# Kernel optimization log

Hardware: AMD Instinct MI355X
Metric: run time of the kernel (lower is better)

Reference implementation:

```python
import jax, jax.numpy as jnp
import numpy as np

IN_CH, OUT_CH, B, H, W = 32, 64, 8, 256, 256
EPS = 1e-5

SOBEL_X = [[1., 0., -1.], [2., 0., -2.], [1., 0., -1.]]
SOBEL_Y = [[1., 2., 1.], [0., 0., 0.], [-1., -2., -1.]]
LAP = [[0., 1., 0.], [1., -4., 1.], [0., 1., 0.]]

DN = ('NCHW', 'OIHW', 'NCHW')


def conv2d(x, w, b, pad, groups=1):
    y = jax.lax.conv_general_dilated(x, w, (1, 1), [(pad, pad), (pad, pad)],
                                     dimension_numbers=DN, feature_group_count=groups)
    return y + b[None, :, None, None]


def dw_conv(x, k2d):
    # fixed depthwise 3x3 conv, groups=C, padding=1, no bias
    c = x.shape[1]
    kern = jnp.tile(jnp.asarray(k2d, x.dtype)[None, None], (c, 1, 1, 1))  # (C,1,3,3)
    return jax.lax.conv_general_dilated(x, kern, (1, 1), [(1, 1), (1, 1)],
                                        dimension_numbers=DN, feature_group_count=c)


def bn4d(x, p):  # eval-mode BN; x (B,C,H,W), p (4,C) = gamma, beta, mean, var
    g, b, m, v = p
    s = g * jax.lax.rsqrt(v + EPS)
    return (x - m[None, :, None, None]) * s[None, :, None, None] + b[None, :, None, None]


def bn2d(h, p):  # h (B,C)
    g, b, m, v = p
    return (h - m) * (g * jax.lax.rsqrt(v + EPS)) + b


def _bn_params(key, c):
    k1, k2, k3, k4 = jax.random.split(key, 4)
    g = 1.0 + 0.1 * jax.random.normal(k1, (c,), jnp.float32)
    b = 0.1 * jax.random.normal(k2, (c,), jnp.float32)
    m = 0.1 * jax.random.normal(k3, (c,), jnp.float32)
    v = jax.random.uniform(k4, (c,), jnp.float32, 0.5, 1.5)
    return jnp.stack([g, b, m, v])


def setup_inputs() -> dict:
    key = jax.random.key(0)
    ks = jax.random.split(key, 24)
    s = 0.05
    return {
        'x': jax.random.normal(ks[0], (B, IN_CH, H, W), jnp.float32),
        'gate_w1': s * jax.random.normal(ks[1], (IN_CH, IN_CH), jnp.float32),
        'gate_b1': s * jax.random.normal(ks[2], (IN_CH,), jnp.float32),
        'gate_bn': _bn_params(ks[3], IN_CH),
        'gate_w2': s * jax.random.normal(ks[4], (3, IN_CH), jnp.float32),
        'gate_b2': s * jax.random.normal(ks[5], (3,), jnp.float32),
        'mw1': s * jax.random.normal(ks[6], (OUT_CH, IN_CH, 3, 3), jnp.float32),
        'mb1': s * jax.random.normal(ks[7], (OUT_CH,), jnp.float32),
        'mbn1': _bn_params(ks[8], OUT_CH),
        'mw2': s * jax.random.normal(ks[9], (OUT_CH, OUT_CH, 5, 5), jnp.float32),
        'mb2': s * jax.random.normal(ks[10], (OUT_CH,), jnp.float32),
        'mbn2': _bn_params(ks[11], OUT_CH),
        'sxw': s * jax.random.normal(ks[12], (OUT_CH, IN_CH, 5, 5), jnp.float32),
        'sxb': s * jax.random.normal(ks[13], (OUT_CH,), jnp.float32),
        'sxbn': _bn_params(ks[14], OUT_CH),
        'syw': s * jax.random.normal(ks[15], (OUT_CH, IN_CH, 5, 5), jnp.float32),
        'syb': s * jax.random.normal(ks[16], (OUT_CH,), jnp.float32),
        'sybn': _bn_params(ks[17], OUT_CH),
        'lw': s * jax.random.normal(ks[18], (OUT_CH, IN_CH, 5, 5), jnp.float32),
        'lb': s * jax.random.normal(ks[19], (OUT_CH,), jnp.float32),
        'lbn': _bn_params(ks[20], OUT_CH),
    }


def reference(x, gate_w1, gate_b1, gate_bn, gate_w2, gate_b2,
              mw1, mb1, mbn1, mw2, mb2, mbn2,
              sxw, sxb, sxbn, syw, syb, sybn, lw, lb, lbn):
    # gate: GAP -> 1x1 conv -> BN -> tanh -> 1x1 conv -> top-1 one-hot over 3 experts
    gap = x.mean((2, 3))                                   # (B, C_in)
    h = jnp.tanh(bn2d(gap @ gate_w1.T + gate_b1, gate_bn))
    k = h @ gate_w2.T + gate_b2                            # (B, 3)
    oh = jax.nn.one_hot(jnp.argmax(k, axis=1), 3, dtype=x.dtype)  # (B, 3)

    # expert 0: main branch (conv3x3+BN+ReLU -> conv5x5+BN+ReLU)
    main = jax.nn.relu(bn4d(conv2d(x, mw1, mb1, 1), mbn1))
    main = jax.nn.relu(bn4d(conv2d(main, mw2, mb2, 2), mbn2))

    # expert 1: mean of sobel-x and sobel-y branches
    sx = jax.nn.relu(bn4d(conv2d(dw_conv(x, SOBEL_X), sxw, sxb, 2), sxbn))
    sy = jax.nn.relu(bn4d(conv2d(dw_conv(x, SOBEL_Y), syw, syb, 2), sybn))
    sobel = (sx + sy) * 0.5

    # expert 2: laplacian branch
    lap = jax.nn.relu(bn4d(conv2d(dw_conv(x, LAP), lw, lb, 2), lbn))

    # one-hot gated combination (== stack + one_hot mask + sum in the original)
    w = oh[:, :, None, None, None]  # (B, 3, 1, 1, 1)
    return main * w[:, 0] + sobel * w[:, 1] + lap * w[:, 2]
```

## Files before the change

kernel.cpp:

```cpp
#include <hip/hip_runtime.h>

#define BB 8
#define IC 32
#define OC 64
#define HH 256
#define WW 256
#define EPS 1e-5f

typedef __attribute__((ext_vector_type(8))) short bf16x8;
typedef __attribute__((ext_vector_type(4))) float f32x4;

#define XSTR 40
#define YSTR 40

#define WS_GAP   0
#define WS_BIDX  256
#define WS_W1F   264
#define WS_B1F   (WS_W1F + 9216)
#define WS_W2F   (WS_B1F + 64)
#define WS_B2F   (WS_W2F + 51200)
#define WS_SXWT  (WS_B2F + 64)
#define WS_SXBF  (WS_SXWT + 51200)
#define WS_SYWT  (WS_SXBF + 64)
#define WS_SYBF  (WS_SYWT + 51200)
#define WS_LWT   (WS_SYBF + 64)
#define WS_LBF   (WS_LWT + 51200)

__device__ inline unsigned short bf16r(float f) {
    unsigned int u = __float_as_uint(f);
    unsigned int r = (u + 0x7fffu + ((u >> 16) & 1u)) >> 16;
    return (unsigned short)r;
}

__global__ void prep_kernel(const float* __restrict__ mw1, const float* __restrict__ mb1, const float* __restrict__ mbn1,
                            const float* __restrict__ mw2, const float* __restrict__ mb2, const float* __restrict__ mbn2,
                            const float* __restrict__ sxw, const float* __restrict__ sxb, const float* __restrict__ sxbn,
                            const float* __restrict__ syw, const float* __restrict__ syb, const float* __restrict__ sybn,
                            const float* __restrict__ lw,  const float* __restrict__ lb,  const float* __restrict__ lbn,
                            float* __restrict__ ws) {
    int idx = blockIdx.x * 256 + threadIdx.x;

    if (idx < 18432) {
        int j = idx & 7, lane = (idx >> 3) & 63, oct = (idx >> 9) & 1, ht = idx >> 10;
        int t = ht % 9, h = ht / 9;
        int oc = h * 32 + oct * 16 + (lane & 15);
        int ic = (lane >> 4) * 8 + j;
        float s = mbn1[oc] * rsqrtf(mbn1[192 + oc] + EPS);
        ((unsigned short*)(ws + WS_W1F))[idx] = bf16r(mw1[(oc * IC + ic) * 9 + t] * s);
    }
    if (idx < 102400) {
        int j = idx & 7, lane = (idx >> 3) & 63, oct = (idx >> 9) & 3, ht = idx >> 11;
        int t = ht % 25, h = ht / 25;
        int oc = oct * 16 + (lane & 15);
        int ic = h * 32 + (lane >> 4) * 8 + j;
        float s = mbn2[oc] * rsqrtf(mbn2[192 + oc] + EPS);
        ((unsigned short*)(ws + WS_W2F))[idx] = bf16r(mw2[(oc * OC + ic) * 25 + t] * s);
    }
    if (idx < 51200) {
        int oc = idx & 63, k = (idx >> 6) % 25, ic = idx / (25 * 64);
        float ssx = sxbn[oc] * rsqrtf(sxbn[192 + oc] + EPS);
        float ssy = sybn[oc] * rsqrtf(sybn[192 + oc] + EPS);
        float sl  = lbn[oc]  * rsqrtf(lbn[192 + oc]  + EPS);
        ws[WS_SXWT + idx] = sxw[(oc * IC + ic) * 25 + k] * ssx;
        ws[WS_SYWT + idx] = syw[(oc * IC + ic) * 25 + k] * ssy;
        ws[WS_LWT  + idx] = lw [(oc * IC + ic) * 25 + k] * sl;
    }
    if (idx < 64) {
        float s1 = mbn1[idx] * rsqrtf(mbn1[192 + idx] + EPS);
        ws[WS_B1F + idx] = (mb1[idx] - mbn1[128 + idx]) * s1 + mbn1[64 + idx];
        float s2 = mbn2[idx] * rsqrtf(mbn2[192 + idx] + EPS);
        ws[WS_B2F + idx] = (mb2[idx] - mbn2[128 + idx]) * s2 + mbn2[64 + idx];
        float sx = sxbn[idx] * rsqrtf(sxbn[192 + idx] + EPS);
        ws[WS_SXBF + idx] = (sxb[idx] - sxbn[128 + idx]) * sx + sxbn[64 + idx];
        float sy = sybn[idx] * rsqrtf(sybn[192 + idx] + EPS);
        ws[WS_SYBF + idx] = (syb[idx] - sybn[128 + idx]) * sy + sybn[64 + idx];
        float sl = lbn[idx] * rsqrtf(lbn[192 + idx] + EPS);
        ws[WS_LBF + idx] = (lb[idx] - lbn[128 + idx]) * sl + lbn[64 + idx];
    }
}

__global__ void gap_kernel(const float* __restrict__ x, float* __restrict__ ws) {
    int bc = blockIdx.x;
    const float4* p = (const float4*)(x + (size_t)bc * (HH * WW));
    float s = 0.f;
    for (int i = threadIdx.x; i < (HH * WW) / 4; i += 256) {
        float4 v = p[i];
        s += (v.x + v.y) + (v.z + v.w);
    }
    #pragma unroll
    for (int off = 32; off; off >>= 1) s += __shfl_down(s, off, 64);
    __shared__ float red[4];
    int lane = threadIdx.x & 63, w = threadIdx.x >> 6;
    if (lane == 0) red[w] = s;
    __syncthreads();
    if (threadIdx.x == 0)
        ws[WS_GAP + bc] = (red[0] + red[1] + red[2] + red[3]) * (1.f / (HH * WW));
}

__global__ void gate_kernel(const float* __restrict__ w1, const float* __restrict__ b1,
                            const float* __restrict__ gbn,
                            const float* __restrict__ w2, const float* __restrict__ b2,
                            float* __restrict__ ws) {
    __shared__ float hsh[8][32];
    int tid = threadIdx.x;
    int b = tid >> 5, j = tid & 31;
    float acc = b1[j];
    for (int i = 0; i < 32; i++) acc += ws[WS_GAP + b * 32 + i] * w1[j * 32 + i];
    float s = gbn[j] * rsqrtf(gbn[96 + j] + EPS);
    hsh[b][j] = tanhf((acc - gbn[64 + j]) * s + gbn[32 + j]);
    __syncthreads();
    if (tid < 8) {
        float best = -1e30f; int bi = 0;
        for (int c = 0; c < 3; c++) {
            float k = b2[c];
            for (int jj = 0; jj < 32; jj++) k += hsh[tid][jj] * w2[c * 32 + jj];
            if (k > best) { best = k; bi = c; }
        }
        ((int*)ws)[WS_BIDX + tid] = bi;
    }
}

__global__ void __launch_bounds__(256, 2)
main_kernel(const float* __restrict__ x, const float* __restrict__ ws, float* __restrict__ out) {
    __shared__ __align__(16) short xs[484 * XSTR];
    __shared__ __align__(16) short ys[400 * YSTR];

    int b = blockIdx.y;
    if (((const int*)ws)[WS_BIDX + b] != 0) return;
    int tile = blockIdx.x;
    int ty = (tile >> 4) * 16, tx = (tile & 15) * 16;
    int tid = threadIdx.x;
    int w = tid >> 6, lane = tid & 63, n = lane & 15, quad = lane >> 4;

    const float* xb = x + (size_t)b * IC * HH * WW;
    for (int p = tid; p < 484; p += 256) {
        int rr = p / 22, cc = p % 22;
        int gy = ty - 3 + rr, gx = tx - 3 + cc;
        bool v = ((unsigned)gy < HH) && ((unsigned)gx < WW);
        const float* xp = xb + gy * WW + gx;
        short* dst = xs + p * XSTR;
        #pragma unroll
        for (int ic = 0; ic < IC; ic += 4) {
            float f0 = v ? xp[(size_t)(ic + 0) * (HH * WW)] : 0.f;
            float f1 = v ? xp[(size_t)(ic + 1) * (HH * WW)] : 0.f;
            float f2 = v ? xp[(size_t)(ic + 2) * (HH * WW)] : 0.f;
            float f3 = v ? xp[(size_t)(ic + 3) * (HH * WW)] : 0.f;
            uint2 pk;
            pk.x = (unsigned int)bf16r(f0) | ((unsigned int)bf16r(f1) << 16);
            pk.y = (unsigned int)bf16r(f2) | ((unsigned int)bf16r(f3) << 16);
            *(uint2*)(dst + ic) = pk;
        }
    }

    const short* w1v = (const short*)(ws + WS_W1F);
    const bf16x8* w2v = (const bf16x8*)(ws + WS_W2F);

    f32x4 acc2[4][4];
    #pragma unroll
    for (int i = 0; i < 4; i++)
        #pragma unroll
        for (int jj = 0; jj < 4; jj++) acc2[i][jj] = (f32x4){0.f, 0.f, 0.f, 0.f};
    int mrow0 = w * 4;
    int yr0   = w * 5;

    __syncthreads();

    #pragma unroll 1
    for (int h = 0; h < 2; h++) {
        if (h) __syncthreads();

        #pragma unroll
        for (int cg = 0; cg < 2; cg++) {
            int cb = cg * 4;
            f32x4 a1[5][2];
            #pragma unroll
            for (int rr = 0; rr < 5; rr++) {
                a1[rr][0] = (f32x4){0.f, 0.f, 0.f, 0.f};
                a1[rr][1] = (f32x4){0.f, 0.f, 0.f, 0.f};
            }
            #pragma unroll
            for (int dw = 0; dw < 3; dw++) {
                bf16x8 w1f[3][2];
                #pragma unroll
                for (int dh = 0; dh < 3; dh++) {
                    int t = dh * 3 + dw;
                    w1f[dh][0] = *(const bf16x8*)(w1v + (((h * 9 + t) * 2 + 0) * 64 + lane) * 8);
                    w1f[dh][1] = *(const bf16x8*)(w1v + (((h * 9 + t) * 2 + 1) * 64 + lane) * 8);
                }
                bf16x8 bfr[7];
                #pragma unroll
                for (int rI = 0; rI < 7; rI++)
                    bfr[rI] = *(const bf16x8*)(xs + ((yr0 + rI) * 22 + cb + n + dw) * XSTR + quad * 8);
                #pragma unroll
                for (int dh = 0; dh < 3; dh++)
                    #pragma unroll
                    for (int rr = 0; rr < 5; rr++) {
                        a1[rr][0] = __builtin_amdgcn_mfma_f32_16x16x32_bf16(w1f[dh][0], bfr[rr + dh], a1[rr][0], 0, 0, 0);
                        a1[rr][1] = __builtin_amdgcn_mfma_f32_16x16x32_bf16(w1f[dh][1], bfr[rr + dh], a1[rr][1], 0, 0, 0);
                    }
            }
            #pragma unroll
            for (int oct = 0; oct < 2; oct++) {
                float bias1[4];
                #pragma unroll
                for (int r = 0; r < 4; r++)
                    bias1[r] = ws[WS_B1F + h * 32 + oct * 16 + quad * 4 + r];
                #pragma unroll
                for (int rr = 0; rr < 5; rr++) {
                    int yr = yr0 + rr;
                    int gy2 = ty - 2 + yr, gx2 = tx - 2 + cb + n;
                    bool inb = ((unsigned)gy2 < HH) && ((unsigned)gx2 < WW);
                    float v0 = inb ? fmaxf(a1[rr][oct][0] + bias1[0], 0.f) : 0.f;
                    float v1 = inb ? fmaxf(a1[rr][oct][1] + bias1[1], 0.f) : 0.f;
                    float v2 = inb ? fmaxf(a1[rr][oct][2] + bias1[2], 0.f) : 0.f;
                    float v3 = inb ? fmaxf(a1[rr][oct][3] + bias1[3], 0.f) : 0.f;
                    uint2 pk;
                    pk.x = (unsigned int)bf16r(v0) | ((unsigned int)bf16r(v1) << 16);
                    pk.y = (unsigned int)bf16r(v2) | ((unsigned int)bf16r(v3) << 16);
                    *(uint2*)(ys + (yr * 20 + cb + n) * YSTR + oct * 16 + quad * 4) = pk;
                }
            }
        }
        __syncthreads();

        const bf16x8* w2h = w2v + (size_t)h * 100 * 64;
        bf16x8 af[4];
        {
            int base = 0 * 64 + lane;
            af[0] = w2h[base]; af[1] = w2h[base + 64]; af[2] = w2h[base + 128]; af[3] = w2h[base + 192];
        }
        bf16x8 bfr2[8];
        #pragma unroll
        for (int k = 0; k < 25; k++) {
            int dw = k / 5, dh = k % 5;
            if (dh == 0) {
                #pragma unroll
                for (int rI = 0; rI < 8; rI++)
                    bfr2[rI] = *(const bf16x8*)(ys + ((mrow0 + rI) * 20 + n + dw) * YSTR + quad * 8);
            }
            bf16x8 an[4];
            if (k < 24) {
                int kk = k + 1;
                int tn = (kk % 5) * 5 + (kk / 5);
                int base = tn * 4 * 64 + lane;
                an[0] = w2h[base]; an[1] = w2h[base + 64]; an[2] = w2h[base + 128]; an[3] = w2h[base + 192];
            }
            #pragma unroll
            for (int r4 = 0; r4 < 4; r4++) {
                bf16x8 bb = bfr2[r4 + dh];
                acc2[r4][0] = __builtin_amdgcn_mfma_f32_16x16x32_bf16(af[0], bb, acc2[r4][0], 0, 0, 0);
                acc2[r4][1] = __builtin_amdgcn_mfma_f32_16x16x32_bf16(af[1], bb, acc2[r4][1], 0, 0, 0);
                acc2[r4][2] = __builtin_amdgcn_mfma_f32_16x16x32_bf16(af[2], bb, acc2[r4][2], 0, 0, 0);
                acc2[r4][3] = __builtin_amdgcn_mfma_f32_16x16x32_bf16(af[3], bb, acc2[r4][3], 0, 0, 0);
            }
            af[0] = an[0]; af[1] = an[1]; af[2] = an[2]; af[3] = an[3];
        }
    }

    float bias2[4][4];
    #pragma unroll
    for (int oct = 0; oct < 4; oct++)
        #pragma unroll
        for (int r = 0; r < 4; r++)
            bias2[oct][r] = ws[WS_B2F + oct * 16 + quad * 4 + r];

    float* ob = out + (size_t)b * OC * HH * WW;
    #pragma unroll
    for (int r4 = 0; r4 < 4; r4++) {
        int orow = mrow0 + r4;
        #pragma unroll
        for (int oct = 0; oct < 4; oct++) {
            #pragma unroll
            for (int r = 0; r < 4; r++) {
                int oc = oct * 16 + quad * 4 + r;
                float v = fmaxf(acc2[r4][oct][r] + bias2[oct][r], 0.f);
                ob[(size_t)oc * (HH * WW) + (ty + orow) * WW + tx + n] = v;
            }
        }
    }
}

template <int KID>
__global__ void __launch_bounds__(256, 2)
edge_kernel(const float* __restrict__ x, const float* __restrict__ ws, float* __restrict__ out,
            int want, float scale, int accumulate, int wt_off, int bf_off) {
    constexpr float KSX[9] = {1, 0, -1, 2, 0, -2, 1, 0, -1};
    constexpr float KSY[9] = {1, 2, 1, 0, 0, 0, -1, -2, -1};
    constexpr float KLP[9] = {0, 1, 0, 1, -4, 1, 0, 1, 0};

    __shared__ float xsf[8 * 484];
    __shared__ float ysf[8 * 400];
    int b = blockIdx.y;
    if (((const int*)ws)[WS_BIDX + b] != want) return;
    int tile = blockIdx.x;
    int ty = (tile >> 4) * 16, tx = (tile & 15) * 16;
    int tid = threadIdx.x;

    const float* xb = x + (size_t)b * IC * HH * WW;
    const float* wt = ws + wt_off;
    const float* bf = ws + bf_off;

    float acc[8][8];
    #pragma unroll
    for (int o = 0; o < 8; o++)
        #pragma unroll
        for (int j = 0; j < 8; j++) acc[o][j] = 0.f;

    int ocg = tid >> 5;
    int ps  = tid & 31;
    int row = ps >> 1, c0 = (ps & 1) * 8;

    for (int icc = 0; icc < 4; icc++) {
        if (icc) __syncthreads();
        for (int i = tid; i < 8 * 484; i += 256) {
            int ch = i / 484, rem = i % 484, rr = rem / 22, cc = rem % 22;
            int ic = icc * 8 + ch;
            int gy = ty - 3 + rr, gx = tx - 3 + cc;
            float v = 0.f;
            if ((unsigned)gy < HH && (unsigned)gx < WW) v = xb[(size_t)ic * HH * WW + gy * WW + gx];
            xsf[i] = v;
        }
        __syncthreads();
        for (int p = tid; p < 400; p += 256) {
            int r = p / 20, c = p % 20;
            bool inb = ((unsigned)(ty - 2 + r) < HH) && ((unsigned)(tx - 2 + c) < WW);
            #pragma unroll
            for (int ch = 0; ch < 8; ch++) {
                const float* xp = xsf + ch * 484 + r * 22 + c;
                float v = 0.f;
                #pragma unroll
                for (int k = 0; k < 9; k++) {
                    float kv = (KID == 0) ? KSX[k] : (KID == 1) ? KSY[k] : KLP[k];
                    if (kv != 0.f) v += kv * xp[(k / 3) * 22 + (k % 3)];
                }
                ysf[ch * 400 + p] = inb ? v : 0.f;
            }
        }
        __syncthreads();
        for (int ic8 = 0; ic8 < 8; ic8++) {
            const float* yc = ysf + ic8 * 400;
            const float* wbase = wt + ((icc * 8 + ic8) * 25) * 64 + ocg * 8;
            #pragma unroll
            for (int dh = 0; dh < 5; dh++) {
                #pragma unroll
                for (int dw = 0; dw < 5; dw++) {
                    const float* yp = yc + (row + dh) * 20 + c0 + dw;
                    float yv[8];
                    #pragma unroll
                    for (int j = 0; j < 8; j++) yv[j] = yp[j];
                    const float4* wp = (const float4*)(wbase + (dh * 5 + dw) * 64);
                    float4 wa = wp[0], wb = wp[1];
                    float wr[8] = {wa.x, wa.y, wa.z, wa.w, wb.x, wb.y, wb.z, wb.w};
                    #pragma unroll
                    for (int o = 0; o < 8; o++)
                        #pragma unroll
                        for (int j = 0; j < 8; j++) acc[o][j] += wr[o] * yv[j];
                }
            }
        }
    }
    float* ob = out + (size_t)b * OC * HH * WW;
    #pragma unroll
    for (int o = 0; o < 8; o++) {
        int oc = ocg * 8 + o;
        float bb = bf[oc];
        float* op = ob + (size_t)oc * HH * WW + (ty + row) * WW + tx + c0;
        if (accumulate) {
            #pragma unroll
            for (int j = 0; j < 8; j++) op[j] += scale * fmaxf(acc[o][j] + bb, 0.f);
        } else {
            #pragma unroll
            for (int j = 0; j < 8; j++) op[j] = scale * fmaxf(acc[o][j] + bb, 0.f);
        }
    }
}

extern "C" void kernel_launch(void* const* d_in, const int* in_sizes, int n_in,
                              void* d_out, int out_size, void* d_ws, size_t ws_size,
                              hipStream_t stream) {
    const float* x    = (const float*)d_in[0];
    const float* gw1  = (const float*)d_in[1];
    const float* gb1  = (const float*)d_in[2];
    const float* gbn  = (const float*)d_in[3];
    const float* gw2  = (const float*)d_in[4];
    const float* gb2  = (const float*)d_in[5];
    const float* mw1  = (const float*)d_in[6];
    const float* mb1  = (const float*)d_in[7];
    const float* mbn1 = (const float*)d_in[8];
    const float* mw2  = (const float*)d_in[9];
    const float* mb2  = (const float*)d_in[10];
    const float* mbn2 = (const float*)d_in[11];
    const float* sxw  = (const float*)d_in[12];
    const float* sxb  = (const float*)d_in[13];
    const float* sxbn = (const float*)d_in[14];
    const float* syw  = (const float*)d_in[15];
    const float* syb  = (const float*)d_in[16];
    const float* sybn = (const float*)d_in[17];
    const float* lw   = (const float*)d_in[18];
    const float* lb   = (const float*)d_in[19];
    const float* lbn  = (const float*)d_in[20];
    float* ws  = (float*)d_ws;
    float* out = (float*)d_out;

    prep_kernel<<<400, 256, 0, stream>>>(mw1, mb1, mbn1, mw2, mb2, mbn2,
                                         sxw, sxb, sxbn, syw, syb, sybn, lw, lb, lbn, ws);
    gap_kernel<<<256, 256, 0, stream>>>(x, ws);
    gate_kernel<<<1, 256, 0, stream>>>(gw1, gb1, gbn, gw2, gb2, ws);

    dim3 grid(256, BB);
    main_kernel<<<grid, 256, 0, stream>>>(x, ws, out);
    edge_kernel<0><<<grid, 256, 0, stream>>>(x, ws, out, 1, 0.5f, 0, WS_SXWT, WS_SXBF);
    edge_kernel<1><<<grid, 256, 0, stream>>>(x, ws, out, 1, 0.5f, 1, WS_SYWT, WS_SYBF);
    edge_kernel<2><<<grid, 256, 0, stream>>>(x, ws, out, 2, 1.0f, 0, WS_LWT, WS_LBF);
}
```

Baseline: 426.4 us.

## Process four horizontal tiles per block with register-prefetched input halo

The main-branch kernel now gives each block a 16x64 strip, looping over four 16x16 tiles instead of one tile per block. The next tile's input halo is loaded with float4 global loads into registers while the current tile's MFMA conv runs, then converted to bf16 and written to shared memory after the stores. This is meant to hide global-load latency and replace the strided scalar halo loads with vectorized ones. The cost is a grid four times smaller (64x8 blocks), fewer blocks to fill the GPU, and more register pressure from the 17 float4 prefetch buffers.

```diff
diff --git a/kernel.cpp b/kernel.cpp
--- a/kernel.cpp
+++ b/kernel.cpp
@@ -12,6 +12,7 @@
 
 #define XSTR 40
 #define YSTR 40
+#define NT4  4224
 
 #define WS_GAP   0
 #define WS_BIDX  256
@@ -120,6 +121,43 @@
     }
 }
 
+__device__ __forceinline__ void pf_load_range(const float* __restrict__ xb, int ty, int tx,
+                                              int tid, int k0, int k1, float4* pf) {
+    #pragma unroll
+    for (int k = k0; k < k1; k++) {
+        int u = tid + k * 256;
+        if (u < NT4) {
+            int c4 = u % 6, icr = (u / 6) % 32, row = u / 192;
+            int gy = ty - 3 + row, gxb = tx - 4 + c4 * 4;
+            bool valid = ((unsigned)gy < HH) && ((unsigned)gxb < WW);
+            size_t off = valid ? ((size_t)icr * (HH * WW) + gy * WW + gxb) : 0;
+            pf[k - k0] = *(const float4*)(xb + off);
+        }
+    }
+}
+
+__device__ __forceinline__ void xs_write_range(short* __restrict__ xs, int ty, int tx,
+                                               int tid, int k0, int k1, const float4* pf) {
+    #pragma unroll
+    for (int k = k0; k < k1; k++) {
+        int u = tid + k * 256;
+        if (u < NT4) {
+            int c4 = u % 6, icr = (u / 6) % 32, row = u / 192;
+            int gy = ty - 3 + row, gxb = tx - 4 + c4 * 4;
+            bool valid = ((unsigned)gy < HH) && ((unsigned)gxb < WW);
+            float4 v = pf[k - k0];
+            float e0 = valid ? v.x : 0.f, e1 = valid ? v.y : 0.f;
+            float e2 = valid ? v.z : 0.f, e3 = valid ? v.w : 0.f;
+            int ccb = c4 * 4 - 1;
+            short* base = xs + (row * 22) * XSTR + icr;
+            if (c4 != 0) base[(ccb + 0) * XSTR] = (short)bf16r(e0);
+            base[(ccb + 1) * XSTR] = (short)bf16r(e1);
+            base[(ccb + 2) * XSTR] = (short)bf16r(e2);
+            if (c4 != 5) base[(ccb + 3) * XSTR] = (short)bf16r(e3);
+        }
+    }
+}
+
 __global__ void __launch_bounds__(256, 2)
 main_kernel(const float* __restrict__ x, const float* __restrict__ ws, float* __restrict__ out) {
     __shared__ __align__(16) short xs[484 * XSTR];
@@ -127,156 +165,162 @@
 
     int b = blockIdx.y;
     if (((const int*)ws)[WS_BIDX + b] != 0) return;
-    int tile = blockIdx.x;
-    int ty = (tile >> 4) * 16, tx = (tile & 15) * 16;
+    int q = blockIdx.x;
+    int ty  = (q >> 2) * 16;
+    int tx0 = (q & 3) * 64;
     int tid = threadIdx.x;
     int w = tid >> 6, lane = tid & 63, n = lane & 15, quad = lane >> 4;
 
     const float* xb = x + (size_t)b * IC * HH * WW;
-    for (int p = tid; p < 484; p += 256) {
-        int rr = p / 22, cc = p % 22;
-        int gy = ty - 3 + rr, gx = tx - 3 + cc;
-        bool v = ((unsigned)gy < HH) && ((unsigned)gx < WW);
-        const float* xp = xb + gy * WW + gx;
-        short* dst = xs + p * XSTR;
-        #pragma unroll
-        for (int ic = 0; ic < IC; ic += 4) {
-            float f0 = v ? xp[(size_t)(ic + 0) * (HH * WW)] : 0.f;
-            float f1 = v ? xp[(size_t)(ic + 1) * (HH * WW)] : 0.f;
-            float f2 = v ? xp[(size_t)(ic + 2) * (HH * WW)] : 0.f;
-            float f3 = v ? xp[(size_t)(ic + 3) * (HH * WW)] : 0.f;
-            uint2 pk;
-            pk.x = (unsigned int)bf16r(f0) | ((unsigned int)bf16r(f1) << 16);
-            pk.y = (unsigned int)bf16r(f2) | ((unsigned int)bf16r(f3) << 16);
-            *(uint2*)(dst + ic) = pk;
-        }
-    }
-
     const short* w1v = (const short*)(ws + WS_W1F);
     const bf16x8* w2v = (const bf16x8*)(ws + WS_W2F);
 
-    f32x4 acc2[4][4];
-    #pragma unroll
-    for (int i = 0; i < 4; i++)
-        #pragma unroll
-        for (int jj = 0; jj < 4; jj++) acc2[i][jj] = (f32x4){0.f, 0.f, 0.f, 0.f};
+    float4 pfA[8], pfB[9];
+
+    pf_load_range(xb, ty, tx0, tid, 0, 8, pfA);
+    pf_load_range(xb, ty, tx0, tid, 8, 17, pfB);
+    xs_write_range(xs, ty, tx0, tid, 0, 8, pfA);
+    xs_write_range(xs, ty, tx0, tid, 8, 17, pfB);
+    __syncthreads();
+
     int mrow0 = w * 4;
     int yr0   = w * 5;
 
-    __syncthreads();
-
     #pragma unroll 1
-    for (int h = 0; h < 2; h++) {
-        if (h) __syncthreads();
-
+    for (int t = 0; t < 4; t++) {
+        int tx = tx0 + t * 16;
+
+        f32x4 acc2[4][4];
         #pragma unroll
-        for (int cg = 0; cg < 2; cg++) {
-            int cb = cg * 4;
-            f32x4 a1[5][2];
-            #pragma unroll
-            for (int rr = 0; rr < 5; rr++) {
-                a1[rr][0] = (f32x4){0.f, 0.f, 0.f, 0.f};
-                a1[rr][1] = (f32x4){0.f, 0.f, 0.f, 0.f};
-            }
-            #pragma unroll
-            for (int dw = 0; dw < 3; dw++) {
-                bf16x8 w1f[3][2];
-                #pragma unroll
-                for (int dh = 0; dh < 3; dh++) {
-                    int t = dh * 3 + dw;
-                    w1f[dh][0] = *(const bf16x8*)(w1v + (((h * 9 + t) * 2 + 0) * 64 + lane) * 8);
-                    w1f[dh][1] = *(const bf16x8*)(w1v + (((h * 9 + t) * 2 + 1) * 64 + lane) * 8);
-                }
-                bf16x8 bfr[7];
-                #pragma unroll
-                for (int rI = 0; rI < 7; rI++)
-                    bfr[rI] = *(const bf16x8*)(xs + ((yr0 + rI) * 22 + cb + n + dw) * XSTR + quad * 8);
-                #pragma unroll
-                for (int dh = 0; dh < 3; dh++)
+        for (int i = 0; i < 4; i++)
+            #pragma unroll
+            for (int jj = 0; jj < 4; jj++) acc2[i][jj] = (f32x4){0.f, 0.f, 0.f, 0.f};
+
+        #pragma unroll
+        for (int h = 0; h < 2; h++) {
+            #pragma unroll
+            for (int cg = 0; cg < 2; cg++) {
+                int cb = cg * 4;
+                f32x4 a1[5][2];
+                #pragma unroll
+                for (int rr = 0; rr < 5; rr++) {
+                    a1[rr][0] = (f32x4){0.f, 0.f, 0.f, 0.f};
+                    a1[rr][1] = (f32x4){0.f, 0.f, 0.f, 0.f};
+                }
+                #pragma unroll
+                for (int dw = 0; dw < 3; dw++) {
+                    bf16x8 w1f[3][2];
+                    #pragma unroll
+                    for (int dh = 0; dh < 3; dh++) {
+                        int tt = dh * 3 + dw;
+                        w1f[dh][0] = *(const bf16x8*)(w1v + (((h * 9 + tt) * 2 + 0) * 64 + lane) * 8);
+                        w1f[dh][1] = *(const bf16x8*)(w1v + (((h * 9 + tt) * 2 + 1) * 64 + lane) * 8);
+                    }
+                    bf16x8 bfr[7];
+                    #pragma unroll
+                    for (int rI = 0; rI < 7; rI++)
+                        bfr[rI] = *(const bf16x8*)(xs + ((yr0 + rI) * 22 + cb + n + dw) * XSTR + quad * 8);
+                    #pragma unroll
+                    for (int dh = 0; dh < 3; dh++)
+                        #pragma unroll
+                        for (int rr = 0; rr < 5; rr++) {
+                            a1[rr][0] = __builtin_amdgcn_mfma_f32_16x16x32_bf16(w1f[dh][0], bfr[rr + dh], a1[rr][0], 0, 0, 0);
+                            a1[rr][1] = __builtin_amdgcn_mfma_f32_16x16x32_bf16(w1f[dh][1], bfr[rr + dh], a1[rr][1], 0, 0, 0);
+                        }
+                }
+                #pragma unroll
+                for (int oct = 0; oct < 2; oct++) {
+                    float bias1[4];
+                    #pragma unroll
+                    for (int r = 0; r < 4; r++)
+                        bias1[r] = ws[WS_B1F + h * 32 + oct * 16 + quad * 4 + r];
                     #pragma unroll
                     for (int rr = 0; rr < 5; rr++) {
-                        a1[rr][0] = __builtin_amdgcn_mfma_f32_16x16x32_bf16(w1f[dh][0], bfr[rr + dh], a1[rr][0], 0, 0, 0);
-                        a1[rr][1] = __builtin_amdgcn_mfma_f32_16x16x32_bf16(w1f[dh][1], bfr[rr + dh], a1[rr][1], 0, 0, 0);
+                        int yr = yr0 + rr;
+                        int gy2 = ty - 2 + yr, gx2 = tx - 2 + cb + n;
+                        bool inb = ((unsigned)gy2 < HH) && ((unsigned)gx2 < WW);
+                        float v0 = inb ? fmaxf(a1[rr][oct][0] + bias1[0], 0.f) : 0.f;
+                        float v1 = inb ? fmaxf(a1[rr][oct][1] + bias1[1], 0.f) : 0.f;
+                        float v2 = inb ? fmaxf(a1[rr][oct][2] + bias1[2], 0.f) : 0.f;
+                        float v3 = inb ? fmaxf(a1[rr][oct][3] + bias1[3], 0.f) : 0.f;
+                        uint2 pk;
+                        pk.x = (unsigned int)bf16r(v0) | ((unsigned int)bf16r(v1) << 16);
+                        pk.y = (unsigned int)bf16r(v2) | ((unsigned int)bf16r(v3) << 16);
+                        *(uint2*)(ys + (yr * 20 + cb + n) * YSTR + oct * 16 + quad * 4) = pk;
                     }
-            }
-            #pragma unroll
-            for (int oct = 0; oct < 2; oct++) {
-                float bias1[4];
+                }
+            }
+            __syncthreads();
+
+            if (t < 3) {
+                if (h == 0) pf_load_range(xb, ty, tx + 16, tid, 0, 8, pfA);
+                else        pf_load_range(xb, ty, tx + 16, tid, 8, 17, pfB);
+            }
+
+            const bf16x8* w2h = w2v + (size_t)h * 100 * 64;
+            bf16x8 af[4];
+            {
+                int base = lane;
+                af[0] = w2h[base]; af[1] = w2h[base + 64]; af[2] = w2h[base + 128]; af[3] = w2h[base + 192];
+            }
+            bf16x8 bfr2[8];
+            #pragma unroll
+            for (int k = 0; k < 25; k++) {
+                int dw = k / 5, dh = k % 5;
+                if (dh == 0) {
+                    #pragma unroll
+                    for (int rI = 0; rI < 8; rI++)
+                        bfr2[rI] = *(const bf16x8*)(ys + ((mrow0 + rI) * 20 + n + dw) * YSTR + quad * 8);
+                }
+                bf16x8 an[4];
+                if (k < 24) {
+                    int kk = k + 1;
+                    int tn = (kk % 5) * 5 + (kk / 5);
+                    int base = tn * 4 * 64 + lane;
+                    an[0] = w2h[base]; an[1] = w2h[base + 64]; an[2] = w2h[base + 128]; an[3] = w2h[base + 192];
+                }
+                #pragma unroll
+                for (int r4 = 0; r4 < 4; r4++) {
+                    bf16x8 bb = bfr2[r4 + dh];
+                    acc2[r4][0] = __builtin_amdgcn_mfma_f32_16x16x32_bf16(af[0], bb, acc2[r4][0], 0, 0, 0);
+                    acc2[r4][1] = __builtin_amdgcn_mfma_f32_16x16x32_bf16(af[1], bb, acc2[r4][1], 0, 0, 0);
+                    acc2[r4][2] = __builtin_amdgcn_mfma_f32_16x16x32_bf16(af[2], bb, acc2[r4][2], 0, 0, 0);
+                    acc2[r4][3] = __builtin_amdgcn_mfma_f32_16x16x32_bf16(af[3], bb, acc2[r4][3], 0, 0, 0);
+                }
+                af[0] = an[0]; af[1] = an[1]; af[2] = an[2]; af[3] = an[3];
+            }
+            if (h == 0) __syncthreads();
+        }
+
+        {
+            float bias2[4][4];
+            #pragma unroll
+            for (int oct = 0; oct < 4; oct++)
                 #pragma unroll
                 for (int r = 0; r < 4; r++)
-                    bias1[r] = ws[WS_B1F + h * 32 + oct * 16 + quad * 4 + r];
-                #pragma unroll
-                for (int rr = 0; rr < 5; rr++) {
-                    int yr = yr0 + rr;
-                    int gy2 = ty - 2 + yr, gx2 = tx - 2 + cb + n;
-                    bool inb = ((unsigned)gy2 < HH) && ((unsigned)gx2 < WW);
-                    float v0 = inb ? fmaxf(a1[rr][oct][0] + bias1[0], 0.f) : 0.f;
-                    float v1 = inb ? fmaxf(a1[rr][oct][1] + bias1[1], 0.f) : 0.f;
-                    float v2 = inb ? fmaxf(a1[rr][oct][2] + bias1[2], 0.f) : 0.f;
-                    float v3 = inb ? fmaxf(a1[rr][oct][3] + bias1[3], 0.f) : 0.f;
-                    uint2 pk;
-                    pk.x = (unsigned int)bf16r(v0) | ((unsigned int)bf16r(v1) << 16);
-                    pk.y = (unsigned int)bf16r(v2) | ((unsigned int)bf16r(v3) << 16);
-                    *(uint2*)(ys + (yr * 20 + cb + n) * YSTR + oct * 16 + quad * 4) = pk;
-                }
-            }
+                    bias2[oct][r] = ws[WS_B2F + oct * 16 + quad * 4 + r];
+
+            float* ob = out + (size_t)b * OC * HH * WW;
+            #pragma unroll
+            for (int r4 = 0; r4 < 4; r4++) {
+                int orow = mrow0 + r4;
+                #pragma unroll
+                for (int oct = 0; oct < 4; oct++) {
+                    #pragma unroll
+                    for (int r = 0; r < 4; r++) {
+                        int oc = oct * 16 + quad * 4 + r;
+                        float v = fmaxf(acc2[r4][oct][r] + bias2[oct][r], 0.f);
+                        ob[(size_t)oc * (HH * WW) + (ty + orow) * WW + tx + n] = v;
+                    }
+                }
+            }
+        }
+
+        if (t < 3) {
+            xs_write_range(xs, ty, tx + 16, tid, 0, 8, pfA);
+            xs_write_range(xs, ty, tx + 16, tid, 8, 17, pfB);
         }
         __syncthreads();
-
-        const bf16x8* w2h = w2v + (size_t)h * 100 * 64;
-        bf16x8 af[4];
-        {
-            int base = 0 * 64 + lane;
-            af[0] = w2h[base]; af[1] = w2h[base + 64]; af[2] = w2h[base + 128]; af[3] = w2h[base + 192];
-        }
-        bf16x8 bfr2[8];
-        #pragma unroll
-        for (int k = 0; k < 25; k++) {
-            int dw = k / 5, dh = k % 5;
-            if (dh == 0) {
-                #pragma unroll
-                for (int rI = 0; rI < 8; rI++)
-                    bfr2[rI] = *(const bf16x8*)(ys + ((mrow0 + rI) * 20 + n + dw) * YSTR + quad * 8);
-            }
-            bf16x8 an[4];
-            if (k < 24) {
-                int kk = k + 1;
-                int tn = (kk % 5) * 5 + (kk / 5);
-                int base = tn * 4 * 64 + lane;
-                an[0] = w2h[base]; an[1] = w2h[base + 64]; an[2] = w2h[base + 128]; an[3] = w2h[base + 192];
-            }
-            #pragma unroll
-            for (int r4 = 0; r4 < 4; r4++) {
-                bf16x8 bb = bfr2[r4 + dh];
-                acc2[r4][0] = __builtin_amdgcn_mfma_f32_16x16x32_bf16(af[0], bb, acc2[r4][0], 0, 0, 0);
-                acc2[r4][1] = __builtin_amdgcn_mfma_f32_16x16x32_bf16(af[1], bb, acc2[r4][1], 0, 0, 0);
-                acc2[r4][2] = __builtin_amdgcn_mfma_f32_16x16x32_bf16(af[2], bb, acc2[r4][2], 0, 0, 0);
-                acc2[r4][3] = __builtin_amdgcn_mfma_f32_16x16x32_bf16(af[3], bb, acc2[r4][3], 0, 0, 0);
-            }
-            af[0] = an[0]; af[1] = an[1]; af[2] = an[2]; af[3] = an[3];
-        }
-    }
-
-    float bias2[4][4];
-    #pragma unroll
-    for (int oct = 0; oct < 4; oct++)
-        #pragma unroll
-        for (int r = 0; r < 4; r++)
-            bias2[oct][r] = ws[WS_B2F + oct * 16 + quad * 4 + r];
-
-    float* ob = out + (size_t)b * OC * HH * WW;
-    #pragma unroll
-    for (int r4 = 0; r4 < 4; r4++) {
-        int orow = mrow0 + r4;
-        #pragma unroll
-        for (int oct = 0; oct < 4; oct++) {
-            #pragma unroll
-            for (int r = 0; r < 4; r++) {
-                int oc = oct * 16 + quad * 4 + r;
-                float v = fmaxf(acc2[r4][oct][r] + bias2[oct][r], 0.f);
-                ob[(size_t)oc * (HH * WW) + (ty + orow) * WW + tx + n] = v;
-            }
-        }
     }
 }
 
@@ -407,8 +451,9 @@
     gap_kernel<<<256, 256, 0, stream>>>(x, ws);
     gate_kernel<<<1, 256, 0, stream>>>(gw1, gb1, gbn, gw2, gb2, ws);
 
+    dim3 grid_main(64, BB);
+    main_kernel<<<grid_main, 256, 0, stream>>>(x, ws, out);
     dim3 grid(256, BB);
-    main_kernel<<<grid, 256, 0, stream>>>(x, ws, out);
     edge_kernel<0><<<grid, 256, 0, stream>>>(x, ws, out, 1, 0.5f, 0, WS_SXWT, WS_SXBF);
     edge_kernel<1><<<grid, 256, 0, stream>>>(x, ws, out, 1, 0.5f, 1, WS_SYWT, WS_SYBF);
     edge_kernel<2><<<grid, 256, 0, stream>>>(x, ws, out, 2, 1.0f, 0, WS_LWT, WS_LBF);
```

After: 1.272 ms. +198.3%, slower.
